# Kernel tuning notes

Hardware: AMD Instinct MI355X
Metric: run time of the kernel (lower is better)

The kernel has to match this reference:

```python
import math
import jax
import jax.numpy as jnp
import numpy as np

B = 64          # graphs per batch
NPG = 1000      # nodes per graph
IN = 64         # input feature dim
H = 128         # hidden dim
DEG = 16        # avg degree
C = 10          # num classes
RATIO = 0.8     # topk ratio
EPS = 1e-5      # batchnorm eps
E = B * NPG * DEG


def setup_inputs() -> dict:
    key = jax.random.key(0)
    ks = jax.random.split(key, 16)
    x = jax.random.normal(ks[0], (B * NPG, IN), jnp.float32)
    # per-graph random edges, then offset to global node ids
    src = jax.random.randint(ks[1], (B, NPG * DEG), 0, NPG)
    dst = jax.random.randint(ks[2], (B, NPG * DEG), 0, NPG)
    off = (jnp.arange(B) * NPG)[:, None]
    edge_index = jnp.stack([(src + off).reshape(-1), (dst + off).reshape(-1)]).astype(jnp.int32)
    batch = jnp.repeat(jnp.arange(B), NPG).astype(jnp.int32)
    edge_weight = jax.random.uniform(ks[3], (E,), jnp.float32)
    # parameters: block 1 conv is [IN,H]; blocks 2-6 are [H,H] (stacked)
    conv1_w = jax.random.normal(ks[4], (IN, H), jnp.float32) * 0.05
    conv_w = jax.random.normal(ks[5], (5, H, H), jnp.float32) * 0.05
    conv_b = jnp.zeros((6, H), jnp.float32)
    bn_gamma = jnp.ones((6, H), jnp.float32)
    bn_beta = jnp.zeros((6, H), jnp.float32)
    bn_mean = jax.random.normal(ks[6], (6, H), jnp.float32) * 0.01
    bn_var = jax.random.uniform(ks[7], (6, H), jnp.float32, 0.5, 1.5)
    pool_w = jax.random.normal(ks[8], (6, H), jnp.float32)
    d1_w = jax.random.normal(ks[9], (2 * H, 4 * H), jnp.float32) * 0.05
    d1_b = jnp.zeros((4 * H,), jnp.float32)
    d2_w = jax.random.normal(ks[10], (4 * H, C), jnp.float32) * 0.05
    d2_b = jnp.zeros((C,), jnp.float32)
    return dict(x=x, edge_index=edge_index, batch=batch, edge_weight=edge_weight,
                conv1_w=conv1_w, conv_w=conv_w, conv_b=conv_b,
                bn_gamma=bn_gamma, bn_beta=bn_beta, bn_mean=bn_mean, bn_var=bn_var,
                pool_w=pool_w, d1_w=d1_w, d1_b=d1_b, d2_w=d2_w, d2_b=d2_b)


def _gcn_conv(h, src, dst, w_e, W, b, n_nodes):
    # PyG GCNConv: add self-loops (weight 1), sym-normalize, aggregate at dst
    xw = h @ W                                        # [N, H]
    deg = jnp.zeros((n_nodes,), h.dtype).at[dst].add(w_e) + 1.0
    dinv = jax.lax.rsqrt(deg)
    coef = dinv[src] * dinv[dst] * w_e                # [E]
    out = jnp.zeros_like(xw).at[dst].add(coef[:, None] * xw[src])
    out = out + (dinv * dinv)[:, None] * xw + b       # self-loop term + bias
    return out


def reference(x, edge_index, batch, edge_weight, conv1_w, conv_w, conv_b,
              bn_gamma, bn_beta, bn_mean, bn_var, pool_w, d1_w, d1_b, d2_w, d2_b):
    src, dst = edge_index[0], edge_index[1]
    w_e = edge_weight
    h = x
    n_cur = NPG
    flats = jnp.zeros((B, 2 * H), x.dtype)
    for i in range(6):
        N = B * n_cur
        W = conv1_w if i == 0 else conv_w[i - 1]
        hc = _gcn_conv(h, src, dst, w_e, W, conv_b[i], N)
        # BatchNorm (inference) + ReLU
        hc = (hc - bn_mean[i]) * (bn_gamma[i] * jax.lax.rsqrt(bn_var[i] + EPS)) + bn_beta[i]
        hc = jax.nn.relu(hc)
        # TopKPooling: score = tanh(x.w/||w||), keep top ceil(ratio*n) per graph
        pw = pool_w[i]
        score = jnp.tanh(hc @ pw / jnp.linalg.norm(pw))   # [N]
        k = math.ceil(RATIO * n_cur)
        vals, idx = jax.lax.top_k(score.reshape(B, n_cur), k)  # [B,k]
        perm = (idx + (jnp.arange(B) * n_cur)[:, None]).reshape(-1)
        h = hc[perm] * vals.reshape(-1, 1)                # [B*k, H]
        # remap/filter edges; dead edges become (0,0) with weight 0
        inv = jnp.full((N,), -1, jnp.int32).at[perm].set(jnp.arange(B * k, dtype=jnp.int32))
        ok = (inv[src] >= 0) & (inv[dst] >= 0)
        src = jnp.where(ok, inv[src], 0)
        dst = jnp.where(ok, inv[dst], 0)
        w_e = jnp.where(ok, w_e, 0.0)
        n_cur = k
        hb = h.reshape(B, k, H)
        flats = flats + jnp.concatenate([hb.mean(axis=1), hb.max(axis=1)], axis=-1)
    # MLP head (dropout is identity in eval)
    hd = jax.nn.relu(flats @ d1_w + d1_b)
    return hd @ d2_w + d2_b
```

## Files before the change

kernel.cpp:

```cpp
#include <hip/hip_runtime.h>
#include <float.h>
#include <math.h>

#define NGR 64
#define NPG0 1000
#define HDIM 128
#define EG 16000
#define NE (NGR*EG)
#define RPS 1008
#define BNEPS 1e-5f
#define POOL_NB 16

typedef short short8 __attribute__((ext_vector_type(8)));
typedef float f4v __attribute__((ext_vector_type(4)));

__global__ __launch_bounds__(256) void k_wsplit(const float* __restrict__ c1w,
    const float* __restrict__ cw, const float* __restrict__ pw,
    unsigned short* __restrict__ wh, unsigned short* __restrict__ wl,
    float* __restrict__ invnorm){
  int l = blockIdx.x, t = threadIdx.x;
  __shared__ float red[2];
  if(t < 128){
    float v = pw[l*HDIM + t];
    float s = v*v;
    #pragma unroll
    for(int o=32;o>0;o>>=1) s += __shfl_down(s, o, 64);
    if((t & 63)==0) red[t>>6] = s;
  }
  __syncthreads();
  if(t==0) invnorm[l] = 1.0f / sqrtf(red[0]+red[1]);
  int K  = (l==0) ? 64 : 128;
  int sh = (l==0) ? 6 : 7;
  const float* src = (l==0) ? c1w : (cw + (size_t)(l-1)*16384);
  int tot = 128*K;
  for(int o=t;o<tot;o+=256){
    int c = o >> sh, k = o & (K-1);
    float f = src[k*128 + c];
    unsigned u  = __float_as_uint(f);
    unsigned uh = (u + 0x7fffu + ((u>>16)&1u)) & 0xffff0000u;
    float r = f - __uint_as_float(uh);
    unsigned v = __float_as_uint(r);
    int o2 = (k>>3)*1024 + c*8 + (k&7);
    wh[(size_t)l*16384 + o2] = (unsigned short)(uh>>16);
    wl[(size_t)l*16384 + o2] = (unsigned short)((v + 0x7fffu + ((v>>16)&1u))>>16);
  }
}

__global__ __launch_bounds__(256) void k_count0(const int* __restrict__ dst,
    const float* __restrict__ we, int* __restrict__ pcnt, float* __restrict__ pdeg){
  int g = blockIdx.x >> 2, sub = blockIdx.x & 3, t = threadIdx.x;
  __shared__ int   cnt[NPG0];
  __shared__ float degl[NPG0];
  for(int i=t;i<NPG0;i+=256){ cnt[i]=0; degl[i]=0.f; }
  __syncthreads();
  int base = g*EG + sub*4000;
  for(int idx=t; idx<4000; idx+=256){
    int e = base + idx;
    int ld = dst[e] - g*NPG0;
    atomicAdd(&cnt[ld], 1);
    atomicAdd(&degl[ld], we[e]);
  }
  __syncthreads();
  int p = blockIdx.x * NPG0;
  for(int i=t;i<NPG0;i+=256){ pcnt[p+i] = cnt[i]; pdeg[p+i] = degl[i]; }
}

__global__ __launch_bounds__(1024) void k_build(const int* __restrict__ pcnt,
    const float* __restrict__ pdeg, const int* __restrict__ src,
    const int* __restrict__ dst, const float* __restrict__ we,
    int* __restrict__ rp, float* __restrict__ dinvz, float* __restrict__ gsc,
    long long* __restrict__ ec){
  int g = blockIdx.x, t = threadIdx.x;
  __shared__ int sc[2][1024];
  __shared__ int cur[NPG0];
  int c = 0;
  if(t < NPG0){
    c = pcnt[(g*4+0)*NPG0+t] + pcnt[(g*4+1)*NPG0+t]
      + pcnt[(g*4+2)*NPG0+t] + pcnt[(g*4+3)*NPG0+t];
    float dg = pdeg[(g*4+0)*NPG0+t] + pdeg[(g*4+1)*NPG0+t]
             + pdeg[(g*4+2)*NPG0+t] + pdeg[(g*4+3)*NPG0+t];
    float dv = 1.0f / sqrtf(dg + 1.0f);
    dinvz[g*NPG0+t] = dv;
    gsc[g*NPG0+t]   = dv;
  }
  sc[0][t] = c;
  __syncthreads();
  int buf = 0;
  for(int d=1; d<1024; d<<=1){
    int v = sc[buf][t];
    if(t>=d) v += sc[buf][t-d];
    sc[buf^1][t] = v;
    __syncthreads();
    buf ^= 1;
  }
  if(t<=NPG0) rp[g*RPS+t] = (t==0) ? 0 : sc[buf][t-1];
  if(t<NPG0)  cur[t]      = (t==0) ? 0 : sc[buf][t-1];
  __syncthreads();
  int base = g*EG;
  for(int idx=t; idx<EG; idx+=1024){
    int e = base + idx;
    int ld = dst[e] - g*NPG0;
    int pos = atomicAdd(&cur[ld], 1);
    ec[(size_t)base + pos] = (((long long)__float_as_int(we[e]))<<32) | (unsigned)src[e];
  }
}

__device__ inline void bfsplit(float f, unsigned short &h, unsigned short &l){
  unsigned u  = __float_as_uint(f);
  unsigned uh = (u + 0x7fffu + ((u>>16)&1u)) & 0xffff0000u;
  float r = f - __uint_as_float(uh);
  unsigned v = __float_as_uint(r);
  h = (unsigned short)(uh>>16);
  l = (unsigned short)((v + 0x7fffu + ((v>>16)&1u))>>16);
}

template<int KIN>
__global__ __launch_bounds__(256) void k_fused(const int* __restrict__ olist,
    const int* __restrict__ rp, const long long* __restrict__ ec,
    const float* __restrict__ dinvz, const float* __restrict__ gsc,
    const float* __restrict__ h,
    const unsigned short* __restrict__ Wh, const unsigned short* __restrict__ Wl,
    const float* __restrict__ bias, const float* __restrict__ gamma,
    const float* __restrict__ beta, const float* __restrict__ mean,
    const float* __restrict__ var, const float* __restrict__ pw,
    const float* __restrict__ invn_p, float* __restrict__ hout,
    float* __restrict__ score){
  constexpr int L0 = (KIN==64);
  __shared__ __attribute__((aligned(16))) unsigned short AsH[16*KIN];
  __shared__ __attribute__((aligned(16))) unsigned short AsL[16*KIN];
  __shared__ float sp[16][4];
  int t = threadIdx.x;
  int nb = gridDim.x, b = blockIdx.x;
  int q = nb >> 3, r = nb & 7;
  int xcd = b & 7, boff = b >> 3;
  int tile = (xcd < r) ? (xcd*(q+1) + boff) : (r*(q+1) + (xcd-r)*q + boff);
  int r0 = tile * 16;
  const int lane = t & 63, wid = t >> 6;
  const int qw = lane >> 4, sl16 = lane & 15;

  {
    int local = wid*4 + qw;
    int row = r0 + local;
    int d = L0 ? row : olist[row];
    int g = d / NPG0;
    int ld = d - g*NPG0;
    int e0 = rp[g*RPS+ld], e1 = rp[g*RPS+ld+1];
    float dvd = dinvz[d];
    float gsd = gsc[d];
    float4 a0; a0.x=0.f; a0.y=0.f; a0.z=0.f; a0.w=0.f;
    float4 a1; a1.x=0.f; a1.y=0.f; a1.z=0.f; a1.w=0.f;
    for(int b2=e0;b2<e1;b2+=16){
      int mm = e1-b2; if(mm>16) mm=16;
      long long rec = (sl16<mm) ? ec[(size_t)g*EG + b2 + sl16] : 0;
      int   sl = (int)(rec & 0xffffffffLL);
      float cl = __int_as_float((int)(rec>>32)) * gsc[sl];
      long long pk = (((long long)__float_as_int(cl))<<32) | (unsigned)sl;
      for(int jj=0;jj<mm;jj++){
        long long p = __shfl(pk, (qw<<4) + jj, 64);
        float c = __int_as_float((int)(p>>32));
        if(c != 0.f){
          int s = (int)(p & 0xffffffffLL);
          if(L0){
            float4 hv = *(const float4*)(h + (size_t)s*64 + 4*sl16);
            a0.x += c*hv.x; a0.y += c*hv.y; a0.z += c*hv.z; a0.w += c*hv.w;
          } else {
            const float4* hp = (const float4*)(h + (size_t)s*HDIM + 8*sl16);
            float4 h0 = hp[0], h1 = hp[1];
            a0.x += c*h0.x; a0.y += c*h0.y; a0.z += c*h0.z; a0.w += c*h0.w;
            a1.x += c*h1.x; a1.y += c*h1.y; a1.z += c*h1.z; a1.w += c*h1.w;
          }
        }
      }
    }
    if(L0){
      float4 hs = *(const float4*)(h + (size_t)d*64 + 4*sl16);
      float4 o;
      o.x = dvd*(a0.x + gsd*hs.x); o.y = dvd*(a0.y + gsd*hs.y);
      o.z = dvd*(a0.z + gsd*hs.z); o.w = dvd*(a0.w + gsd*hs.w);
      ushort4 h4, l4;
      bfsplit(o.x, h4.x, l4.x); bfsplit(o.y, h4.y, l4.y);
      bfsplit(o.z, h4.z, l4.z); bfsplit(o.w, h4.w, l4.w);
      int off2 = (local*128 + sl16*8) ^ ((local&7)<<4);
      *(ushort4*)((char*)AsH + off2) = h4;
      *(ushort4*)((char*)AsL + off2) = l4;
    } else {
      const float4* hp = (const float4*)(h + (size_t)d*HDIM + 8*sl16);
      float4 s0 = hp[0], s1 = hp[1];
      float4 o0, o1;
      o0.x = dvd*(a0.x + gsd*s0.x); o0.y = dvd*(a0.y + gsd*s0.y);
      o0.z = dvd*(a0.z + gsd*s0.z); o0.w = dvd*(a0.w + gsd*s0.w);
      o1.x = dvd*(a1.x + gsd*s1.x); o1.y = dvd*(a1.y + gsd*s1.y);
      o1.z = dvd*(a1.z + gsd*s1.z); o1.w = dvd*(a1.w + gsd*s1.w);
      ushort4 h4, l4;
      int off2 = (local*256 + sl16*16) ^ ((local&7)<<4);
      bfsplit(o0.x, h4.x, l4.x); bfsplit(o0.y, h4.y, l4.y);
      bfsplit(o0.z, h4.z, l4.z); bfsplit(o0.w, h4.w, l4.w);
      *(ushort4*)((char*)AsH + off2) = h4;
      *(ushort4*)((char*)AsL + off2) = l4;
      bfsplit(o1.x, h4.x, l4.x); bfsplit(o1.y, h4.y, l4.y);
      bfsplit(o1.z, h4.z, l4.z); bfsplit(o1.w, h4.w, l4.w);
      *(ushort4*)((char*)AsH + off2 + 8) = h4;
      *(ushort4*)((char*)AsL + off2 + 8) = l4;
    }
  }
  __syncthreads();

  f4v acc[2];
  #pragma unroll
  for(int n=0;n<2;n++){ acc[n][0]=0.f; acc[n][1]=0.f; acc[n][2]=0.f; acc[n][3]=0.f; }
  #pragma unroll
  for(int ks=0; ks<KIN/32; ks++){
    short8 ah, al, bh[2], bl[2];
    int kb = ks*64 + qw*16;
    int panel = ks*4 + qw;
    #pragma unroll
    for(int n=0;n<2;n++){
      int col = wid*32 + n*16 + sl16;
      int goff = (panel*128 + col)*8;
      bh[n] = *(const short8*)(Wh + goff);
      bl[n] = *(const short8*)(Wl + goff);
    }
    {
      int row = sl16;
      int off2 = (row*(KIN*2) + kb) ^ ((row&7)<<4);
      ah = *(const short8*)((const char*)AsH + off2);
      al = *(const short8*)((const char*)AsL + off2);
    }
    #pragma unroll
    for(int n=0;n<2;n++){
      acc[n] = __builtin_amdgcn_mfma_f32_16x16x32_bf16(ah, bh[n], acc[n], 0,0,0);
      acc[n] = __builtin_amdgcn_mfma_f32_16x16x32_bf16(ah, bl[n], acc[n], 0,0,0);
      acc[n] = __builtin_amdgcn_mfma_f32_16x16x32_bf16(al, bh[n], acc[n], 0,0,0);
      acc[n] = __builtin_amdgcn_mfma_f32_16x16x32_bf16(al, bl[n], acc[n], 0,0,0);
    }
  }

  float invn = invn_p[0];
  float bi[2], scv[2], bt[2], mn[2], pv[2];
  #pragma unroll
  for(int n=0;n<2;n++){
    int c = wid*32 + n*16 + sl16;
    bi[n]  = bias[c];
    scv[n] = gamma[c] * (1.0f/sqrtf(var[c] + BNEPS));
    bt[n]  = beta[c];
    mn[n]  = mean[c];
    pv[n]  = pw[c];
  }
  #pragma unroll
  for(int i=0;i<4;i++){
    int rl  = qw*4 + i;
    int row = r0 + rl;
    int orig = olist ? olist[row] : row;
    float p = 0.f;
    #pragma unroll
    for(int n=0;n<2;n++){
      float v = fmaxf((acc[n][i] + bi[n] - mn[n])*scv[n] + bt[n], 0.f);
      hout[(size_t)orig*HDIM + wid*32 + n*16 + sl16] = v;
      p += v*pv[n];
    }
    p += __shfl_xor(p, 1, 64); p += __shfl_xor(p, 2, 64);
    p += __shfl_xor(p, 4, 64); p += __shfl_xor(p, 8, 64);
    if(sl16==0) sp[rl][wid] = p;
  }
  __syncthreads();
  if(t < 16) score[r0 + t] = tanhf(((sp[t][0]+sp[t][1]) + (sp[t][2]+sp[t][3])) * invn);
}

__global__ __launch_bounds__(512) void k_topk(int n, int k,
    const float* __restrict__ score, const int* __restrict__ curlist,
    float* __restrict__ vals, int* __restrict__ nextlist,
    float* __restrict__ dinvz, float* __restrict__ gsc){
  int g = blockIdx.x, t = threadIdx.x;
  __shared__ unsigned keys[1024];
  __shared__ int hist[256];
  __shared__ int ssum[256];
  __shared__ int sc2[2][512];
  __shared__ int eqbuf[1024];
  __shared__ int eqn;
  __shared__ int sh_B, sh_need, sh_E, sh_cut;
  __shared__ unsigned sh_pref;
  for(int i=t;i<n;i+=512){
    unsigned b = __float_as_uint(score[g*n+i]);
    keys[i] = (b & 0x80000000u) ? ~b : (b | 0x80000000u);
  }
  if(t==0){ sh_need = k; sh_pref = 0u; sh_cut = 0x7fffffff; }
  __syncthreads();
  for(int pass=0; pass<4; pass++){
    int shift = 24 - 8*pass;
    if(t<256) hist[t]=0;
    __syncthreads();
    unsigned pref = sh_pref; int need = sh_need;
    for(int i=t;i<n;i+=512){
      unsigned u = keys[i];
      bool m = (pass==0) || ((u >> (shift+8)) == pref);
      if(m) atomicAdd(&hist[(u>>shift)&255], 1);
    }
    __syncthreads();
    if(t<256) ssum[t] = hist[t];
    __syncthreads();
    for(int d=1; d<256; d<<=1){
      int v=0;
      if(t<256) v = ssum[t] + ((t+d<256)? ssum[t+d] : 0);
      __syncthreads();
      if(t<256) ssum[t] = v;
      __syncthreads();
    }
    if(t<256){
      int Sgt = ssum[t] - hist[t];
      if(Sgt < need && need <= ssum[t]) sh_B = t;
    }
    __syncthreads();
    int B = sh_B;
    if(t==0){
      sh_need = need - (ssum[B] - hist[B]);
      sh_pref = (pass==0) ? (unsigned)B : ((pref<<8) | (unsigned)B);
      if(pass==3) sh_E = hist[B];
    }
    __syncthreads();
  }
  unsigned T = sh_pref; int r_eq = sh_need; int E = sh_E;
  if(E > r_eq){
    if(t==0) eqn = 0;
    __syncthreads();
    for(int i=t;i<n;i+=512) if(keys[i]==T){ int p=atomicAdd(&eqn,1); eqbuf[p]=i; }
    __syncthreads();
    if(t==0){
      int last = -1;
      for(int j=0;j<r_eq;j++){
        int mn = 0x7fffffff;
        for(int q2=0;q2<E;q2++){ int v=eqbuf[q2]; if(v>last && v<mn) mn=v; }
        last = mn;
      }
      sh_cut = last;
    }
    __syncthreads();
  }
  int cut = sh_cut;
  int c0=0, c1=0;
  {
    int i=t;
    if(i<n){ unsigned u=keys[i]; c0 = (u>T) || (u==T && i<=cut); }
    i=t+512;
    if(i<n){ unsigned u=keys[i]; c1 = (u>T) || (u==T && i<=cut); }
  }
  sc2[0][t] = c0+c1;
  __syncthreads();
  int buf=0;
  for(int d=1; d<512; d<<=1){
    int v = sc2[buf][t];
    if(t>=d) v += sc2[buf][t-d];
    sc2[buf^1][t]=v;
    __syncthreads();
    buf^=1;
  }
  int base = (t==0) ? 0 : sc2[buf][t-1];
  {
    int i=t;
    if(i<n){
      int orig = curlist ? curlist[g*n+i] : (g*NPG0 + i);
      if(c0){
        unsigned u=keys[i];
        float f = __uint_as_float((u & 0x80000000u) ? (u ^ 0x80000000u) : ~u);
        vals[g*k+base]=f; nextlist[g*k+base]=orig; base++;
      } else { dinvz[orig]=0.f; gsc[orig]=0.f; }
    }
    i=t+512;
    if(i<n){
      int orig = curlist ? curlist[g*n+i] : (g*NPG0 + i);
      if(c1){
        unsigned u=keys[i];
        float f = __uint_as_float((u & 0x80000000u) ? (u ^ 0x80000000u) : ~u);
        vals[g*k+base]=f; nextlist[g*k+base]=orig;
      } else { dinvz[orig]=0.f; gsc[orig]=0.f; }
    }
  }
}

__global__ __launch_bounds__(256) void k_gpd(int k, int do_deg,
    const float* __restrict__ hraw, const float* __restrict__ vals,
    const int* __restrict__ nextlist,
    float* __restrict__ sumst, float* __restrict__ maxst,
    const int* __restrict__ rp, const long long* __restrict__ ec,
    float* __restrict__ dinvz, float* __restrict__ gsc){
  int g = blockIdx.x & 63;
  int chunk = blockIdx.x >> 6;
  int wid = threadIdx.x >> 6, lane = threadIdx.x & 63;
  int ww = chunk*4 + wid;
  const int half = lane >> 5, sl32 = lane & 31;
  const int qw   = lane >> 4, sl16 = lane & 15;
  const int NH = POOL_NB*4*2;
  float4 psum; psum.x=0.f; psum.y=0.f; psum.z=0.f; psum.w=0.f;
  float4 pmax; pmax.x=-FLT_MAX; pmax.y=-FLT_MAX; pmax.z=-FLT_MAX; pmax.w=-FLT_MAX;
  for(int j = ww*2 + half; j < k; j += NH){
    float v = vals[g*k+j];
    int d = nextlist[g*k+j];
    float4 hv = *(const float4*)(hraw + (size_t)d*HDIM + 4*sl32);
    float4 o; o.x=hv.x*v; o.y=hv.y*v; o.z=hv.z*v; o.w=hv.w*v;
    psum.x+=o.x; psum.y+=o.y; psum.z+=o.z; psum.w+=o.w;
    pmax.x=fmaxf(pmax.x,o.x); pmax.y=fmaxf(pmax.y,o.y);
    pmax.z=fmaxf(pmax.z,o.z); pmax.w=fmaxf(pmax.w,o.w);
  }
  if(do_deg){
    const int NQ = POOL_NB*4*4;
    for(int j = ww*4 + qw; j < k; j += NQ){
      int d  = nextlist[g*k + j];
      int ld = d - g*NPG0;
      int e0 = rp[g*RPS+ld], e1 = rp[g*RPS+ld+1];
      float deg = 0.f;
      for(int b=e0+sl16; b<e1; b+=16){
        long long rec = ec[(size_t)g*EG + b];
        int s = (int)(rec & 0xffffffffLL);
        float w = __int_as_float((int)(rec>>32));
        if(dinvz[s] != 0.f) deg += w;
      }
      #pragma unroll
      for(int o=8;o>0;o>>=1) deg += __shfl_xor(deg, o, 64);
      if(sl16==0){
        float dv = 1.0f / sqrtf(deg + 1.0f);
        dinvz[d] = dv;
        gsc[d] = dv * vals[g*k+j];
      }
    }
  }
  psum.x += __shfl_xor(psum.x, 32, 64); psum.y += __shfl_xor(psum.y, 32, 64);
  psum.z += __shfl_xor(psum.z, 32, 64); psum.w += __shfl_xor(psum.w, 32, 64);
  pmax.x = fmaxf(pmax.x, __shfl_xor(pmax.x, 32, 64));
  pmax.y = fmaxf(pmax.y, __shfl_xor(pmax.y, 32, 64));
  pmax.z = fmaxf(pmax.z, __shfl_xor(pmax.z, 32, 64));
  pmax.w = fmaxf(pmax.w, __shfl_xor(pmax.w, 32, 64));
  __shared__ float ss[4][128];
  __shared__ float sm[4][128];
  if(half==0){
    *(float4*)&ss[wid][4*sl32] = psum;
    *(float4*)&sm[wid][4*sl32] = pmax;
  }
  __syncthreads();
  int t = threadIdx.x;
  if(t < 128){
    float s = (ss[0][t]+ss[1][t]) + (ss[2][t]+ss[3][t]);
    float m = fmaxf(fmaxf(sm[0][t], sm[1][t]), fmaxf(sm[2][t], sm[3][t]));
    sumst[(size_t)(chunk*NGR + g)*HDIM + t] = s;
    maxst[(size_t)(chunk*NGR + g)*HDIM + t] = m;
  }
}

__global__ __launch_bounds__(512) void k_head(const float* __restrict__ sumstage,
    const float* __restrict__ maxstage,
    const float* __restrict__ d1w, const float* __restrict__ d1b,
    const float* __restrict__ d2w, const float* __restrict__ d2b, float* __restrict__ out){
  const float kinv[6] = {1.f/800.f, 1.f/640.f, 1.f/512.f, 1.f/410.f, 1.f/328.f, 1.f/263.f};
  int g = blockIdx.x, j = threadIdx.x;
  __shared__ float fl[256];
  __shared__ float hd[512];
  if(j < 128){
    float s = 0.f;
    #pragma unroll
    for(int l=0;l<6;l++){
      float ls = 0.f;
      for(int c=0;c<POOL_NB;c++)
        ls += sumstage[(size_t)((l*POOL_NB + c)*NGR + g)*HDIM + j];
      s += ls * kinv[l];
    }
    fl[j] = s;
  } else if(j < 256){
    int f = j - 128;
    float m = 0.f;
    #pragma unroll
    for(int l=0;l<6;l++){
      float lm = -FLT_MAX;
      for(int c=0;c<POOL_NB;c++)
        lm = fmaxf(lm, maxstage[(size_t)((l*POOL_NB + c)*NGR + g)*HDIM + f]);
      m += lm;
    }
    fl[j] = m;
  }
  __syncthreads();
  float acc = d1b[j];
  for(int i=0;i<256;i++) acc += fl[i]*d1w[i*512+j];
  hd[j] = fmaxf(acc, 0.f);
  __syncthreads();
  if(j < 10){
    float a = d2b[j];
    for(int i=0;i<512;i++) a += hd[i]*d2w[i*10+j];
    out[g*10+j] = a;
  }
}

extern "C" void kernel_launch(void* const* d_in, const int* in_sizes, int n_in,
                              void* d_out, int out_size, void* d_ws, size_t ws_size,
                              hipStream_t stream) {
  const float* x    = (const float*)d_in[0];
  const int* ei     = (const int*)d_in[1];
  const float* ew   = (const float*)d_in[3];
  const float* conv1w = (const float*)d_in[4];
  const float* convw  = (const float*)d_in[5];
  const float* convb  = (const float*)d_in[6];
  const float* bng    = (const float*)d_in[7];
  const float* bnb    = (const float*)d_in[8];
  const float* bnm    = (const float*)d_in[9];
  const float* bnv    = (const float*)d_in[10];
  const float* poolw  = (const float*)d_in[11];
  const float* d1w    = (const float*)d_in[12];
  const float* d1b    = (const float*)d_in[13];
  const float* d2w    = (const float*)d_in[14];
  const float* d2b    = (const float*)d_in[15];
  float* out = (float*)d_out;

  char* w = (char*)d_ws;
  float* hbufA = (float*)w; w += (size_t)64000*128*4;
  float* hbufB = (float*)w; w += (size_t)64000*128*4;
  long long* ec = (long long*)w; w += (size_t)NE*8;
  int*   rp    = (int*)w;   w += (size_t)NGR*RPS*4;
  int*   pcnt  = (int*)w;   w += (size_t)256*NPG0*4;
  float* pdeg  = (float*)w; w += (size_t)256*NPG0*4;
  float* dinvz = (float*)w; w += (size_t)64000*4;
  float* gsc   = (float*)w; w += (size_t)64000*4;
  float* score = (float*)w; w += (size_t)64000*4;
  float* vals  = (float*)w; w += (size_t)51200*4;
  int*   listA = (int*)w;   w += (size_t)51200*4;
  int*   listB = (int*)w;   w += (size_t)51200*4;
  float* invno = (float*)w; w += 64;
  float* sumstage = (float*)w; w += (size_t)6*POOL_NB*NGR*HDIM*4;
  float* maxstage = (float*)w; w += (size_t)6*POOL_NB*NGR*HDIM*4;
  unsigned short* whi = (unsigned short*)w; w += (size_t)6*16384*2;
  unsigned short* wlo = (unsigned short*)w; w += (size_t)6*16384*2;

  k_wsplit<<<6,256,0,stream>>>(conv1w, convw, poolw, whi, wlo, invno);

  const int ns[6]={1000,800,640,512,410,328};
  const int ks[6]={800,640,512,410,328,263};

  k_count0<<<256,256,0,stream>>>(ei+NE, ew, pcnt, pdeg);
  k_build<<<64,1024,0,stream>>>(pcnt, pdeg, ei, ei+NE, ew, rp, dinvz, gsc, ec);

  k_fused<64><<<4000,256,0,stream>>>(nullptr, rp, ec, dinvz, gsc, x, whi, wlo,
                                     convb, bng, bnb, bnm, bnv, poolw, invno,
                                     hbufA, score);
  k_topk<<<64,512,0,stream>>>(1000, 800, score, nullptr, vals, listA, dinvz, gsc);
  k_gpd<<<64*POOL_NB,256,0,stream>>>(800, 1, hbufA, vals, listA,
                                     sumstage, maxstage, rp, ec, dinvz, gsc);

  int* cur = listA; int* nxt = listB;
  float* hin = hbufA; float* hot = hbufB;
  for(int i=1;i<6;i++){
    int n = ns[i], k = ks[i];
    k_fused<128><<<4*n,256,0,stream>>>(cur, rp, ec, dinvz, gsc, hin,
                                       whi + (size_t)i*16384, wlo + (size_t)i*16384,
                                       convb+i*128, bng+i*128, bnb+i*128, bnm+i*128,
                                       bnv+i*128, poolw+i*128, invno+i,
                                       hot, score);
    k_topk<<<64,512,0,stream>>>(n, k, score, cur, vals, nxt, dinvz, gsc);
    k_gpd<<<64*POOL_NB,256,0,stream>>>(k, (i<5)?1:0, hot, vals, nxt,
                                       sumstage + (size_t)i*POOL_NB*NGR*HDIM,
                                       maxstage + (size_t)i*POOL_NB*NGR*HDIM,
                                       rp, ec, dinvz, gsc);
    int* tmp = cur; cur = nxt; nxt = tmp;
    float* htmp = hin; hin = hot; hot = htmp;
  }

  k_head<<<64,512,0,stream>>>(sumstage, maxstage, d1w, d1b, d2w, d2b, out);
}
```

Measured before the change: 423.3 us.

## Process 32 rows per block in fused GCN kernel with interleaved gathers

Doubles the row tile of the fused aggregate+GEMM+BN+score kernel from 16 to 32 rows, halving the grid. Each quarter-wave now gathers neighbor features for two destination rows with interleaved loops, giving more memory-level parallelism. Each wave reuses its loaded weight fragments across two 16-row MFMA tiles. The cost is more registers and LDS per block, fewer blocks, and extra divergence when the two rows have different degrees.

```diff
diff --git a/kernel.cpp b/kernel.cpp
--- a/kernel.cpp
+++ b/kernel.cpp
@@ -126,91 +126,154 @@
     const float* __restrict__ invn_p, float* __restrict__ hout,
     float* __restrict__ score){
   constexpr int L0 = (KIN==64);
-  __shared__ __attribute__((aligned(16))) unsigned short AsH[16*KIN];
-  __shared__ __attribute__((aligned(16))) unsigned short AsL[16*KIN];
-  __shared__ float sp[16][4];
+  __shared__ __attribute__((aligned(16))) unsigned short AsH[32*KIN];
+  __shared__ __attribute__((aligned(16))) unsigned short AsL[32*KIN];
+  __shared__ float sp[32][4];
   int t = threadIdx.x;
   int nb = gridDim.x, b = blockIdx.x;
   int q = nb >> 3, r = nb & 7;
   int xcd = b & 7, boff = b >> 3;
   int tile = (xcd < r) ? (xcd*(q+1) + boff) : (r*(q+1) + (xcd-r)*q + boff);
-  int r0 = tile * 16;
+  int r0 = tile * 32;
   const int lane = t & 63, wid = t >> 6;
   const int qw = lane >> 4, sl16 = lane & 15;
 
   {
-    int local = wid*4 + qw;
-    int row = r0 + local;
-    int d = L0 ? row : olist[row];
-    int g = d / NPG0;
-    int ld = d - g*NPG0;
-    int e0 = rp[g*RPS+ld], e1 = rp[g*RPS+ld+1];
-    float dvd = dinvz[d];
-    float gsd = gsc[d];
-    float4 a0; a0.x=0.f; a0.y=0.f; a0.z=0.f; a0.w=0.f;
-    float4 a1; a1.x=0.f; a1.y=0.f; a1.z=0.f; a1.w=0.f;
-    for(int b2=e0;b2<e1;b2+=16){
-      int mm = e1-b2; if(mm>16) mm=16;
-      long long rec = (sl16<mm) ? ec[(size_t)g*EG + b2 + sl16] : 0;
-      int   sl = (int)(rec & 0xffffffffLL);
-      float cl = __int_as_float((int)(rec>>32)) * gsc[sl];
-      long long pk = (((long long)__float_as_int(cl))<<32) | (unsigned)sl;
-      for(int jj=0;jj<mm;jj++){
-        long long p = __shfl(pk, (qw<<4) + jj, 64);
-        float c = __int_as_float((int)(p>>32));
-        if(c != 0.f){
-          int s = (int)(p & 0xffffffffLL);
-          if(L0){
-            float4 hv = *(const float4*)(h + (size_t)s*64 + 4*sl16);
-            a0.x += c*hv.x; a0.y += c*hv.y; a0.z += c*hv.z; a0.w += c*hv.w;
-          } else {
-            const float4* hp = (const float4*)(h + (size_t)s*HDIM + 8*sl16);
-            float4 h0 = hp[0], h1 = hp[1];
-            a0.x += c*h0.x; a0.y += c*h0.y; a0.z += c*h0.z; a0.w += c*h0.w;
-            a1.x += c*h1.x; a1.y += c*h1.y; a1.z += c*h1.z; a1.w += c*h1.w;
+    int localA = wid*8 + qw;
+    int localB = wid*8 + 4 + qw;
+    int rowA = r0 + localA, rowB = r0 + localB;
+    int dA = L0 ? rowA : olist[rowA];
+    int dB = L0 ? rowB : olist[rowB];
+    int gA = dA / NPG0, gB = dB / NPG0;
+    int e0A = rp[gA*RPS + (dA - gA*NPG0)], e1A = rp[gA*RPS + (dA - gA*NPG0) + 1];
+    int e0B = rp[gB*RPS + (dB - gB*NPG0)], e1B = rp[gB*RPS + (dB - gB*NPG0) + 1];
+    float dvdA = dinvz[dA], gsdA = gsc[dA];
+    float dvdB = dinvz[dB], gsdB = gsc[dB];
+    float4 a0A; a0A.x=0.f; a0A.y=0.f; a0A.z=0.f; a0A.w=0.f;
+    float4 a1A; a1A.x=0.f; a1A.y=0.f; a1A.z=0.f; a1A.w=0.f;
+    float4 a0B; a0B.x=0.f; a0B.y=0.f; a0B.z=0.f; a0B.w=0.f;
+    float4 a1B; a1B.x=0.f; a1B.y=0.f; a1B.z=0.f; a1B.w=0.f;
+    const long long* ecgA = ec + (size_t)gA*EG;
+    const long long* ecgB = ec + (size_t)gB*EG;
+    int bA = e0A, bB = e0B;
+    while(bA < e1A || bB < e1B){
+      int mmA = (bA < e1A) ? ((e1A-bA > 16) ? 16 : (e1A-bA)) : 0;
+      int mmB = (bB < e1B) ? ((e1B-bB > 16) ? 16 : (e1B-bB)) : 0;
+      long long pkA = 0, pkB = 0;
+      if(sl16 < mmA){
+        long long rec = ecgA[bA + sl16];
+        int   sl = (int)(rec & 0xffffffffLL);
+        float cl = __int_as_float((int)(rec>>32)) * gsc[sl];
+        pkA = (((long long)__float_as_int(cl))<<32) | (unsigned)sl;
+      }
+      if(sl16 < mmB){
+        long long rec = ecgB[bB + sl16];
+        int   sl = (int)(rec & 0xffffffffLL);
+        float cl = __int_as_float((int)(rec>>32)) * gsc[sl];
+        pkB = (((long long)__float_as_int(cl))<<32) | (unsigned)sl;
+      }
+      int mr = (mmA > mmB) ? mmA : mmB;
+      for(int jj=0;jj<mr;jj++){
+        if(jj < mmA){
+          long long p = __shfl(pkA, (qw<<4) + jj, 64);
+          float c = __int_as_float((int)(p>>32));
+          if(c != 0.f){
+            int s = (int)(p & 0xffffffffLL);
+            if(L0){
+              float4 hv = *(const float4*)(h + (size_t)s*64 + 4*sl16);
+              a0A.x += c*hv.x; a0A.y += c*hv.y; a0A.z += c*hv.z; a0A.w += c*hv.w;
+            } else {
+              const float4* hp = (const float4*)(h + (size_t)s*HDIM + 8*sl16);
+              float4 h0 = hp[0], h1 = hp[1];
+              a0A.x += c*h0.x; a0A.y += c*h0.y; a0A.z += c*h0.z; a0A.w += c*h0.w;
+              a1A.x += c*h1.x; a1A.y += c*h1.y; a1A.z += c*h1.z; a1A.w += c*h1.w;
+            }
           }
         }
-      }
+        if(jj < mmB){
+          long long p = __shfl(pkB, (qw<<4) + jj, 64);
+          float c = __int_as_float((int)(p>>32));
+          if(c != 0.f){
+            int s = (int)(p & 0xffffffffLL);
+            if(L0){
+              float4 hv = *(const float4*)(h + (size_t)s*64 + 4*sl16);
+              a0B.x += c*hv.x; a0B.y += c*hv.y; a0B.z += c*hv.z; a0B.w += c*hv.w;
+            } else {
+              const float4* hp = (const float4*)(h + (size_t)s*HDIM + 8*sl16);
+              float4 h0 = hp[0], h1 = hp[1];
+              a0B.x += c*h0.x; a0B.y += c*h0.y; a0B.z += c*h0.z; a0B.w += c*h0.w;
+              a1B.x += c*h1.x; a1B.y += c*h1.y; a1B.z += c*h1.z; a1B.w += c*h1.w;
+            }
+          }
+        }
+      }
+      if(mmA) bA += 16;
+      if(mmB) bB += 16;
     }
     if(L0){
-      float4 hs = *(const float4*)(h + (size_t)d*64 + 4*sl16);
-      float4 o;
-      o.x = dvd*(a0.x + gsd*hs.x); o.y = dvd*(a0.y + gsd*hs.y);
-      o.z = dvd*(a0.z + gsd*hs.z); o.w = dvd*(a0.w + gsd*hs.w);
+      float4 hsA = *(const float4*)(h + (size_t)dA*64 + 4*sl16);
+      float4 hsB = *(const float4*)(h + (size_t)dB*64 + 4*sl16);
+      float4 oA, oB;
+      oA.x = dvdA*(a0A.x + gsdA*hsA.x); oA.y = dvdA*(a0A.y + gsdA*hsA.y);
+      oA.z = dvdA*(a0A.z + gsdA*hsA.z); oA.w = dvdA*(a0A.w + gsdA*hsA.w);
+      oB.x = dvdB*(a0B.x + gsdB*hsB.x); oB.y = dvdB*(a0B.y + gsdB*hsB.y);
+      oB.z = dvdB*(a0B.z + gsdB*hsB.z); oB.w = dvdB*(a0B.w + gsdB*hsB.w);
       ushort4 h4, l4;
-      bfsplit(o.x, h4.x, l4.x); bfsplit(o.y, h4.y, l4.y);
-      bfsplit(o.z, h4.z, l4.z); bfsplit(o.w, h4.w, l4.w);
-      int off2 = (local*128 + sl16*8) ^ ((local&7)<<4);
-      *(ushort4*)((char*)AsH + off2) = h4;
-      *(ushort4*)((char*)AsL + off2) = l4;
+      bfsplit(oA.x, h4.x, l4.x); bfsplit(oA.y, h4.y, l4.y);
+      bfsplit(oA.z, h4.z, l4.z); bfsplit(oA.w, h4.w, l4.w);
+      int offA = (localA*128 + sl16*8) ^ ((localA&7)<<4);
+      *(ushort4*)((char*)AsH + offA) = h4;
+      *(ushort4*)((char*)AsL + offA) = l4;
+      bfsplit(oB.x, h4.x, l4.x); bfsplit(oB.y, h4.y, l4.y);
+      bfsplit(oB.z, h4.z, l4.z); bfsplit(oB.w, h4.w, l4.w);
+      int offB = (localB*128 + sl16*8) ^ ((localB&7)<<4);
+      *(ushort4*)((char*)AsH + offB) = h4;
+      *(ushort4*)((char*)AsL + offB) = l4;
     } else {
-      const float4* hp = (const float4*)(h + (size_t)d*HDIM + 8*sl16);
-      float4 s0 = hp[0], s1 = hp[1];
+      const float4* hpA = (const float4*)(h + (size_t)dA*HDIM + 8*sl16);
+      const float4* hpB = (const float4*)(h + (size_t)dB*HDIM + 8*sl16);
+      float4 s0 = hpA[0], s1 = hpA[1];
       float4 o0, o1;
-      o0.x = dvd*(a0.x + gsd*s0.x); o0.y = dvd*(a0.y + gsd*s0.y);
-      o0.z = dvd*(a0.z + gsd*s0.z); o0.w = dvd*(a0.w + gsd*s0.w);
-      o1.x = dvd*(a1.x + gsd*s1.x); o1.y = dvd*(a1.y + gsd*s1.y);
-      o1.z = dvd*(a1.z + gsd*s1.z); o1.w = dvd*(a1.w + gsd*s1.w);
+      o0.x = dvdA*(a0A.x + gsdA*s0.x); o0.y = dvdA*(a0A.y + gsdA*s0.y);
+      o0.z = dvdA*(a0A.z + gsdA*s0.z); o0.w = dvdA*(a0A.w + gsdA*s0.w);
+      o1.x = dvdA*(a1A.x + gsdA*s1.x); o1.y = dvdA*(a1A.y + gsdA*s1.y);
+      o1.z = dvdA*(a1A.z + gsdA*s1.z); o1.w = dvdA*(a1A.w + gsdA*s1.w);
       ushort4 h4, l4;
-      int off2 = (local*256 + sl16*16) ^ ((local&7)<<4);
+      int offA = (localA*256 + sl16*16) ^ ((localA&7)<<4);
       bfsplit(o0.x, h4.x, l4.x); bfsplit(o0.y, h4.y, l4.y);
       bfsplit(o0.z, h4.z, l4.z); bfsplit(o0.w, h4.w, l4.w);
-      *(ushort4*)((char*)AsH + off2) = h4;
-      *(ushort4*)((char*)AsL + off2) = l4;
+      *(ushort4*)((char*)AsH + offA) = h4;
+      *(ushort4*)((char*)AsL + offA) = l4;
       bfsplit(o1.x, h4.x, l4.x); bfsplit(o1.y, h4.y, l4.y);
       bfsplit(o1.z, h4.z, l4.z); bfsplit(o1.w, h4.w, l4.w);
-      *(ushort4*)((char*)AsH + off2 + 8) = h4;
-      *(ushort4*)((char*)AsL + off2 + 8) = l4;
-    }
-  }
-  __syncthreads();
-
-  f4v acc[2];
+      *(ushort4*)((char*)AsH + offA + 8) = h4;
+      *(ushort4*)((char*)AsL + offA + 8) = l4;
+      s0 = hpB[0]; s1 = hpB[1];
+      o0.x = dvdB*(a0B.x + gsdB*s0.x); o0.y = dvdB*(a0B.y + gsdB*s0.y);
+      o0.z = dvdB*(a0B.z + gsdB*s0.z); o0.w = dvdB*(a0B.w + gsdB*s0.w);
+      o1.x = dvdB*(a1B.x + gsdB*s1.x); o1.y = dvdB*(a1B.y + gsdB*s1.y);
+      o1.z = dvdB*(a1B.z + gsdB*s1.z); o1.w = dvdB*(a1B.w + gsdB*s1.w);
+      int offB = (localB*256 + sl16*16) ^ ((localB&7)<<4);
+      bfsplit(o0.x, h4.x, l4.x); bfsplit(o0.y, h4.y, l4.y);
+      bfsplit(o0.z, h4.z, l4.z); bfsplit(o0.w, h4.w, l4.w);
+      *(ushort4*)((char*)AsH + offB) = h4;
+      *(ushort4*)((char*)AsL + offB) = l4;
+      bfsplit(o1.x, h4.x, l4.x); bfsplit(o1.y, h4.y, l4.y);
+      bfsplit(o1.z, h4.z, l4.z); bfsplit(o1.w, h4.w, l4.w);
+      *(ushort4*)((char*)AsH + offB + 8) = h4;
+      *(ushort4*)((char*)AsL + offB + 8) = l4;
+    }
+  }
+  __syncthreads();
+
+  f4v acc[2][2];
   #pragma unroll
-  for(int n=0;n<2;n++){ acc[n][0]=0.f; acc[n][1]=0.f; acc[n][2]=0.f; acc[n][3]=0.f; }
+  for(int m=0;m<2;m++)
+    #pragma unroll
+    for(int n=0;n<2;n++){ acc[m][n][0]=0.f; acc[m][n][1]=0.f; acc[m][n][2]=0.f; acc[m][n][3]=0.f; }
   #pragma unroll
   for(int ks=0; ks<KIN/32; ks++){
-    short8 ah, al, bh[2], bl[2];
+    short8 ah[2], al[2], bh[2], bl[2];
     int kb = ks*64 + qw*16;
     int panel = ks*4 + qw;
     #pragma unroll
@@ -220,18 +283,22 @@
       bh[n] = *(const short8*)(Wh + goff);
       bl[n] = *(const short8*)(Wl + goff);
     }
-    {
-      int row = sl16;
+    #pragma unroll
+    for(int m=0;m<2;m++){
+      int row = m*16 + sl16;
       int off2 = (row*(KIN*2) + kb) ^ ((row&7)<<4);
-      ah = *(const short8*)((const char*)AsH + off2);
-      al = *(const short8*)((const char*)AsL + off2);
-    }
-    #pragma unroll
-    for(int n=0;n<2;n++){
-      acc[n] = __builtin_amdgcn_mfma_f32_16x16x32_bf16(ah, bh[n], acc[n], 0,0,0);
-      acc[n] = __builtin_amdgcn_mfma_f32_16x16x32_bf16(ah, bl[n], acc[n], 0,0,0);
-      acc[n] = __builtin_amdgcn_mfma_f32_16x16x32_bf16(al, bh[n], acc[n], 0,0,0);
-      acc[n] = __builtin_amdgcn_mfma_f32_16x16x32_bf16(al, bl[n], acc[n], 0,0,0);
+      ah[m] = *(const short8*)((const char*)AsH + off2);
+      al[m] = *(const short8*)((const char*)AsL + off2);
+    }
+    #pragma unroll
+    for(int m=0;m<2;m++){
+      #pragma unroll
+      for(int n=0;n<2;n++){
+        acc[m][n] = __builtin_amdgcn_mfma_f32_16x16x32_bf16(ah[m], bh[n], acc[m][n], 0,0,0);
+        acc[m][n] = __builtin_amdgcn_mfma_f32_16x16x32_bf16(ah[m], bl[n], acc[m][n], 0,0,0);
+        acc[m][n] = __builtin_amdgcn_mfma_f32_16x16x32_bf16(al[m], bh[n], acc[m][n], 0,0,0);
+        acc[m][n] = __builtin_amdgcn_mfma_f32_16x16x32_bf16(al[m], bl[n], acc[m][n], 0,0,0);
+      }
     }
   }
 
@@ -247,23 +314,26 @@
     pv[n]  = pw[c];
   }
   #pragma unroll
-  for(int i=0;i<4;i++){
-    int rl  = qw*4 + i;
-    int row = r0 + rl;
-    int orig = olist ? olist[row] : row;
-    float p = 0.f;
-    #pragma unroll
-    for(int n=0;n<2;n++){
-      float v = fmaxf((acc[n][i] + bi[n] - mn[n])*scv[n] + bt[n], 0.f);
-      hout[(size_t)orig*HDIM + wid*32 + n*16 + sl16] = v;
-      p += v*pv[n];
-    }
-    p += __shfl_xor(p, 1, 64); p += __shfl_xor(p, 2, 64);
-    p += __shfl_xor(p, 4, 64); p += __shfl_xor(p, 8, 64);
-    if(sl16==0) sp[rl][wid] = p;
-  }
-  __syncthreads();
-  if(t < 16) score[r0 + t] = tanhf(((sp[t][0]+sp[t][1]) + (sp[t][2]+sp[t][3])) * invn);
+  for(int m=0;m<2;m++){
+    #pragma unroll
+    for(int i=0;i<4;i++){
+      int rl  = m*16 + qw*4 + i;
+      int row = r0 + rl;
+      int orig = olist ? olist[row] : row;
+      float p = 0.f;
+      #pragma unroll
+      for(int n=0;n<2;n++){
+        float v = fmaxf((acc[m][n][i] + bi[n] - mn[n])*scv[n] + bt[n], 0.f);
+        hout[(size_t)orig*HDIM + wid*32 + n*16 + sl16] = v;
+        p += v*pv[n];
+      }
+      p += __shfl_xor(p, 1, 64); p += __shfl_xor(p, 2, 64);
+      p += __shfl_xor(p, 4, 64); p += __shfl_xor(p, 8, 64);
+      if(sl16==0) sp[rl][wid] = p;
+    }
+  }
+  __syncthreads();
+  if(t < 32) score[r0 + t] = tanhf(((sp[t][0]+sp[t][1]) + (sp[t][2]+sp[t][3])) * invn);
 }
 
 __global__ __launch_bounds__(512) void k_topk(int n, int k,
@@ -533,7 +603,7 @@
   k_count0<<<256,256,0,stream>>>(ei+NE, ew, pcnt, pdeg);
   k_build<<<64,1024,0,stream>>>(pcnt, pdeg, ei, ei+NE, ew, rp, dinvz, gsc, ec);
 
-  k_fused<64><<<4000,256,0,stream>>>(nullptr, rp, ec, dinvz, gsc, x, whi, wlo,
+  k_fused<64><<<2000,256,0,stream>>>(nullptr, rp, ec, dinvz, gsc, x, whi, wlo,
                                      convb, bng, bnb, bnm, bnv, poolw, invno,
                                      hbufA, score);
   k_topk<<<64,512,0,stream>>>(1000, 800, score, nullptr, vals, listA, dinvz, gsc);
@@ -544,7 +614,7 @@
   float* hin = hbufA; float* hot = hbufB;
   for(int i=1;i<6;i++){
     int n = ns[i], k = ks[i];
-    k_fused<128><<<4*n,256,0,stream>>>(cur, rp, ec, dinvz, gsc, hin,
+    k_fused<128><<<2*n,256,0,stream>>>(cur, rp, ec, dinvz, gsc, hin,
                                        whi + (size_t)i*16384, wlo + (size_t)i*16384,
                                        convb+i*128, bng+i*128, bnb+i*128, bnm+i*128,
                                        bnv+i*128, poolw+i*128, invno+i,
```

Result: slower. 451.4 us (+6.6%).
